# Kernel tuning notes

Measured on AMD Instinct MI355X. Metric: run time of the kernel, lower is better.

The kernel has to match this reference:

```python
import jax, jax.numpy as jnp
import numpy as np

B, S, T = 512, 1024, 48

def setup_inputs() -> dict:
    key = jax.random.key(0)
    k1, k2, k3, k4, k5 = jax.random.split(key, 5)
    emissions = jax.random.normal(k1, (B, S, T), dtype=jnp.float32)
    tags = jax.random.randint(k2, (B, S), 0, T, dtype=jnp.int32)
    mask = jnp.ones((B, S), dtype=jnp.float32)
    transitions = jax.random.normal(k3, (T, T), dtype=jnp.float32)
    start_transitions = jax.random.normal(k4, (T,), dtype=jnp.float32)
    end_transitions = jax.random.normal(k5, (T,), dtype=jnp.float32)
    return {"emissions": emissions, "tags": tags, "mask": mask,
            "transitions": transitions, "start_transitions": start_transitions,
            "end_transitions": end_transitions}

def _crf_loss(emissions, transitions, start_transitions, end_transitions, tags, mask):
    # ---- numerator: score of the gold path (fully vectorized over seq) ----
    emit = jnp.take_along_axis(emissions, tags[..., None], axis=2)[..., 0]  # (B,S)
    trans = transitions[tags[:, 1:], tags[:, :-1]]                          # (B,S-1)
    lengths = jnp.sum(mask, axis=1).astype(jnp.int32)
    last_idx = jnp.clip(lengths - 1, 0)
    last_tags = jnp.take_along_axis(tags, last_idx[:, None], axis=1)[:, 0]
    numerator = (start_transitions[tags[:, 0]] + emit[:, 0]
                 + jnp.sum(mask[:, 1:] * (emit[:, 1:] + trans), axis=1)
                 + end_transitions[last_tags])                               # (B,)

    # ---- denominator: log-partition via forward algorithm (lax.scan) ----
    def step(score, x):
        em_i, m_i = x  # (B,T), (B,)
        # logsumexp over previous tag; emission is prev-independent so add outside
        nxt = jax.nn.logsumexp(score[:, :, None] + transitions.T[None, :, :], axis=1) + em_i
        score = jnp.where(m_i[:, None] > 0, nxt, score)
        return score, None

    init = start_transitions[None, :] + emissions[:, 0]                      # (B,T)
    xs = (jnp.swapaxes(emissions[:, 1:], 0, 1), jnp.swapaxes(mask[:, 1:], 0, 1))
    final, _ = jax.lax.scan(step, init, xs)
    denominator = jax.nn.logsumexp(final + end_transitions[None, :], axis=1)  # (B,)

    return jnp.mean(denominator - numerator)

def reference(emissions, tags, mask, transitions, start_transitions, end_transitions):
    return _crf_loss(emissions, transitions, start_transitions, end_transitions, tags, mask)
```

## Files before the change

kernel.cpp:

```cpp
#include <hip/hip_runtime.h>
#include <math.h>

#define Bn 512
#define Sn 1024
#define Tn 48
#define NSEG 8
#define SEGLEN 128

typedef _Float16 h4 __attribute__((ext_vector_type(4)));
typedef float    f4 __attribute__((ext_vector_type(4)));

static constexpr float LOG2E = 1.4426950408889634f;
static constexpr float LN2f  = 0.6931471805599453f;

#define MFMA16(A, B, C) __builtin_amdgcn_mfma_f32_16x16x16f16((A), (B), (C), 0, 0, 0)

__global__ __launch_bounds__(512)
void crf_fwd_seg(const float* __restrict__ em,
                 const float* __restrict__ mask,
                 const float* __restrict__ trans,
                 const float* __restrict__ startt,
                 const float* __restrict__ endt,
                 float* __restrict__ den_out)
{
  const int b   = blockIdx.x;
  const int tid = threadIdx.x;
  const int wid = tid >> 6;
  const int l   = tid & 63;
  const int c16 = l & 15;
  const int g   = l >> 4;

  __shared__ __align__(16) float Lm[NSEG][48][49];
  __shared__ __align__(16) float mlds[Sn];
  __shared__ float lwbuf[64];

  const float* __restrict__ emb = em + (size_t)b * Sn * Tn;
  const float* __restrict__ mkb = mask + (size_t)b * Sn;

  if (tid < Sn / 4) *(f4*)&mlds[4 * tid] = *(const f4*)(mkb + 4 * tid);

  h4 Afr[3][3];
  float mtg;
  {
    float tl[3][3][4];
    float mt = -1e30f;
    #pragma unroll
    for (int rt = 0; rt < 3; ++rt)
      #pragma unroll
      for (int kt = 0; kt < 3; ++kt) {
        const f4 t4 = *(const f4*)(trans + (16 * rt + c16) * Tn + 16 * kt + 4 * g);
        #pragma unroll
        for (int i = 0; i < 4; ++i) {
          const float v = t4[i] * LOG2E;
          tl[rt][kt][i] = v;
          mt = fmaxf(mt, v);
        }
      }
    #pragma unroll
    for (int off = 1; off < 64; off <<= 1) mt = fmaxf(mt, __shfl_xor(mt, off));
    mtg = mt;
    #pragma unroll
    for (int rt = 0; rt < 3; ++rt)
      #pragma unroll
      for (int kt = 0; kt < 3; ++kt) {
        h4 r;
        #pragma unroll
        for (int i = 0; i < 4; ++i)
          r[i] = (_Float16)__builtin_amdgcn_exp2f(tl[rt][kt][i] - mtg);
        Afr[rt][kt] = r;
      }
  }

  h4 Bfr[3][3];
  float Mc[3] = {0.f, 0.f, 0.f};
  float cnt = 0.f;
  #pragma unroll
  for (int kt = 0; kt < 3; ++kt)
    #pragma unroll
    for (int ct = 0; ct < 3; ++ct) {
      h4 r;
      #pragma unroll
      for (int i = 0; i < 4; ++i)
        r[i] = (_Float16)(((16 * kt + 4 * g + i) == (16 * ct + c16)) ? 1.0f : 0.0f);
      Bfr[kt][ct] = r;
    }

  auto STEP = [&](const f4& e0, const f4& e1, const f4& e2, float mk,
                  float sc0, float sc1, float sc2,
                  float sh0, float sh1, float sh2) {
    f4 eh[3];
    #pragma unroll
    for (int i = 0; i < 4; ++i) {
      eh[0][i] = __builtin_amdgcn_exp2f(fmaf(e0[i], LOG2E, -6.0f));
      eh[1][i] = __builtin_amdgcn_exp2f(fmaf(e1[i], LOG2E, -6.0f));
      eh[2][i] = __builtin_amdgcn_exp2f(fmaf(e2[i], LOG2E, -6.0f));
    }
    f4 acc[3][3];
    #pragma unroll
    for (int rt = 0; rt < 3; ++rt)
      #pragma unroll
      for (int ct = 0; ct < 3; ++ct) acc[rt][ct] = f4{0.f, 0.f, 0.f, 0.f};
    #pragma unroll
    for (int kt = 0; kt < 3; ++kt)
      #pragma unroll
      for (int rt = 0; rt < 3; ++rt)
        #pragma unroll
        for (int ct = 0; ct < 3; ++ct)
          acc[rt][ct] = MFMA16(Afr[rt][kt], Bfr[kt][ct], acc[rt][ct]);
    const float scv[3] = {sc0, sc1, sc2};
    const float shv[3] = {sh0, sh1, sh2};
    const bool on = (mk > 0.0f);
    #pragma unroll
    for (int rt = 0; rt < 3; ++rt)
      #pragma unroll
      for (int ct = 0; ct < 3; ++ct) {
        h4 nb;
        #pragma unroll
        for (int i = 0; i < 4; ++i)
          nb[i] = (_Float16)(acc[rt][ct][i] * eh[rt][i] * scv[ct]);
        Bfr[rt][ct] = on ? nb : Bfr[rt][ct];
      }
    #pragma unroll
    for (int ct = 0; ct < 3; ++ct) Mc[ct] = fmaf(mk, shv[ct], Mc[ct]);
    cnt += mk;
  };

  auto MEASURE = [&](float (&sh)[3], float (&sc)[3]) {
    #pragma unroll
    for (int ct = 0; ct < 3; ++ct) {
      float m = (float)Bfr[0][ct][0];
      #pragma unroll
      for (int rt = 0; rt < 3; ++rt)
        #pragma unroll
        for (int i = 0; i < 4; ++i) m = fmaxf(m, (float)Bfr[rt][ct][i]);
      m = fmaxf(m, __shfl_xor(m, 16));
      m = fmaxf(m, __shfl_xor(m, 32));
      int eb = ((__float_as_int(m) >> 23) & 0xff) - 127;
      eb = eb < -24 ? -24 : (eb > 40 ? 40 : eb);
      sh[ct] = (float)eb;
      sc[ct] = __int_as_float((127 - eb) << 23);
    }
  };

  auto loadE = [&](int s, f4& x, f4& y, f4& z) {
    const float* p = emb + (size_t)s * Tn + 4 * g;
    x = *(const f4*)(p);
    y = *(const f4*)(p + 16);
    z = *(const f4*)(p + 32);
  };

  __syncthreads();

  const int s_begin = 1 + SEGLEN * wid;
  const int nchunk  = (wid == 7) ? 31 : 32;
  float shP[3] = {0.f, 0.f, 0.f}, scP[3] = {1.f, 1.f, 1.f};
  float shA[3] = {0.f, 0.f, 0.f}, scA[3] = {1.f, 1.f, 1.f};

  f4 E0, E1, E2, N0, N1, N2;
  loadE(s_begin, E0, E1, E2);
  int s = s_begin;
  #pragma unroll 1
  for (int c = 0; c < nchunk; ++c) {
    loadE(s + 1, N0, N1, N2);
    STEP(E0, E1, E2, mlds[s], 1.f, 1.f, 1.f, 0.f, 0.f, 0.f);
    loadE(s + 2, E0, E1, E2);
    STEP(N0, N1, N2, mlds[s + 1], scP[0], scP[1], scP[2], shP[0], shP[1], shP[2]);
    MEASURE(shA, scA);
    loadE(s + 3, N0, N1, N2);
    STEP(E0, E1, E2, mlds[s + 2], 1.f, 1.f, 1.f, 0.f, 0.f, 0.f);
    loadE(s + 4, E0, E1, E2);
    STEP(N0, N1, N2, mlds[s + 3], scA[0], scA[1], scA[2], shA[0], shA[1], shA[2]);
    MEASURE(shP, scP);
    s += 4;
  }
  if (wid == 7) {
    loadE(1022, N0, N1, N2);
    STEP(E0, E1, E2, mlds[1021], 1.f, 1.f, 1.f, 0.f, 0.f, 0.f);
    loadE(1023, E0, E1, E2);
    STEP(N0, N1, N2, mlds[1022], scP[0], scP[1], scP[2], shP[0], shP[1], shP[2]);
    MEASURE(shA, scA);
    STEP(E0, E1, E2, mlds[1023], 1.f, 1.f, 1.f, 0.f, 0.f, 0.f);
  }

  const float addc = (mtg + 6.0f) * cnt;
  #pragma unroll
  for (int kt = 0; kt < 3; ++kt)
    #pragma unroll
    for (int ct = 0; ct < 3; ++ct)
      #pragma unroll
      for (int i = 0; i < 4; ++i)
        Lm[wid][16 * kt + 4 * g + i][16 * ct + c16] =
            __builtin_amdgcn_logf((float)Bfr[kt][ct][i]) + Mc[ct] + addc;
  __syncthreads();

  if (wid == 0) {
    float lw = -INFINITY;
    if (l < Tn) lw = (startt[l] + emb[l]) * LOG2E;
    #pragma unroll 1
    for (int sg = 0; sg < NSEG; ++sg) {
      lwbuf[l] = lw;
      float nlw = lw;
      if (l < Tn) {
        float mj = -INFINITY;
        for (int cc = 0; cc < Tn; ++cc)
          mj = fmaxf(mj, Lm[sg][l][cc] + lwbuf[cc]);
        float ssum = 0.f;
        for (int cc = 0; cc < Tn; ++cc)
          ssum += __builtin_amdgcn_exp2f(Lm[sg][l][cc] + lwbuf[cc] - mj);
        nlw = mj + __builtin_amdgcn_logf(ssum);
      }
      lw = nlw;
    }
    float v = (l < Tn) ? lw + endt[l] * LOG2E : -INFINITY;
    float mv = v;
    #pragma unroll
    for (int off = 32; off; off >>= 1) mv = fmaxf(mv, __shfl_xor(mv, off));
    float zz = (l < Tn) ? __builtin_amdgcn_exp2f(v - mv) : 0.f;
    #pragma unroll
    for (int off = 32; off; off >>= 1) zz += __shfl_xor(zz, off);
    if (l == 0) den_out[b] = (mv + __builtin_amdgcn_logf(zz)) * LN2f;
  }
}

__global__ __launch_bounds__(256) void crf_numer(
    const float* __restrict__ em, const int* __restrict__ tags,
    const float* __restrict__ mask, const float* __restrict__ trans,
    const float* __restrict__ startt, const float* __restrict__ endt,
    float* __restrict__ num_out)
{
  const int b = blockIdx.x, t = threadIdx.x;
  const int*   tgb = tags + (size_t)b * Sn;
  const float* mkb = mask + (size_t)b * Sn;
  const float* emb = em + (size_t)b * Sn * Tn;

  const int s0 = t * 4;
  const int4 tg = *(const int4*)(tgb + s0);
  const f4   mk = *(const f4*)(mkb + s0);
  const int  tprev = (t == 0) ? 0 : tgb[s0 - 1];
  const int  tgarr[5] = {tprev, tg.x, tg.y, tg.z, tg.w};

  float acc  = 0.0f;
  float msum = mk[0] + mk[1] + mk[2] + mk[3];
  #pragma unroll
  for (int i = 0; i < 4; ++i) {
    const int s = s0 + i;
    if (s >= 1)
      acc += mk[i] * (emb[(size_t)s * Tn + tgarr[i + 1]] +
                      trans[tgarr[i + 1] * Tn + tgarr[i]]);
  }
  #pragma unroll
  for (int off = 32; off; off >>= 1) {
    acc  += __shfl_xor(acc, off);
    msum += __shfl_xor(msum, off);
  }
  __shared__ float ra[4], rm[4];
  if ((t & 63) == 0) { ra[t >> 6] = acc; rm[t >> 6] = msum; }
  __syncthreads();
  if (t == 0) {
    const float a = ra[0] + ra[1] + ra[2] + ra[3];
    const float m = rm[0] + rm[1] + rm[2] + rm[3];
    int last = (int)(m + 0.5f) - 1;
    if (last < 0) last = 0;
    const int lt = tgb[last];
    const int t0 = tgb[0];
    num_out[b] = startt[t0] + emb[t0] + a + endt[lt];
  }
}

__global__ __launch_bounds__(512) void reduce_loss(const float* __restrict__ den,
                                                   const float* __restrict__ num,
                                                   float* __restrict__ out) {
  __shared__ float red[8];
  const int t = threadIdx.x;
  float v = den[t] - num[t];
  #pragma unroll
  for (int off = 32; off; off >>= 1) v += __shfl_xor(v, off);
  if ((t & 63) == 0) red[t >> 6] = v;
  __syncthreads();
  if (t == 0) {
    float s = 0.f;
    #pragma unroll
    for (int wv = 0; wv < 8; ++wv) s += red[wv];
    out[0] = s * (1.0f / 512.0f);
  }
}

extern "C" void kernel_launch(void* const* d_in, const int* in_sizes, int n_in,
                              void* d_out, int out_size, void* d_ws, size_t ws_size,
                              hipStream_t stream) {
  const float* emissions = (const float*)d_in[0];
  const int*   tags      = (const int*)d_in[1];
  const float* mask      = (const float*)d_in[2];
  const float* trans     = (const float*)d_in[3];
  const float* startt    = (const float*)d_in[4];
  const float* endt      = (const float*)d_in[5];
  float* den_ws = (float*)d_ws;
  float* num_ws = den_ws + Bn;

  crf_numer<<<Bn, 256, 0, stream>>>(emissions, tags, mask, trans, startt, endt, num_ws);
  crf_fwd_seg<<<Bn, 512, 0, stream>>>(emissions, mask, trans, startt, endt, den_ws);
  reduce_loss<<<1, 512, 0, stream>>>(den_ws, num_ws, (float*)d_out);
}
```

Measured before the change: 256.6 us.

## Precompute fp16 exp-emissions in separate pass and use packed half math in recurrence

```diff
diff --git a/kernel.cpp b/kernel.cpp
--- a/kernel.cpp
+++ b/kernel.cpp
@@ -7,6 +7,7 @@
 #define NSEG 8
 #define SEGLEN 128
 
+typedef _Float16 h2 __attribute__((ext_vector_type(2)));
 typedef _Float16 h4 __attribute__((ext_vector_type(4)));
 typedef float    f4 __attribute__((ext_vector_type(4)));
 
@@ -15,12 +16,50 @@
 
 #define MFMA16(A, B, C) __builtin_amdgcn_mfma_f32_16x16x16f16((A), (B), (C), 0, 0, 0)
 
-__global__ __launch_bounds__(512)
+__device__ __forceinline__ h2 hmax2(h2 a, h2 b) {
+#if __has_builtin(__builtin_elementwise_max)
+  return __builtin_elementwise_max(a, b);
+#else
+  h2 r;
+  r[0] = a[0] > b[0] ? a[0] : b[0];
+  r[1] = a[1] > b[1] ? a[1] : b[1];
+  return r;
+#endif
+}
+__device__ __forceinline__ h2 cvt2(float a, float b) {
+  return __builtin_bit_cast(h2, __builtin_amdgcn_cvt_pkrtz(a, b));
+}
+__device__ __forceinline__ h4 mkh4(h2 lo, h2 hi) {
+  return __builtin_shufflevector(lo, hi, 0, 1, 2, 3);
+}
+__device__ __forceinline__ h2 loh(h4 v) { return __builtin_shufflevector(v, v, 0, 1); }
+__device__ __forceinline__ h2 hih(h4 v) { return __builtin_shufflevector(v, v, 2, 3); }
+
+__global__ __launch_bounds__(256) void ehgen(const float* __restrict__ em,
+                                             _Float16* __restrict__ out) {
+  const size_t total = (size_t)Bn * Sn * Tn;
+  const size_t i = ((size_t)blockIdx.x * 256 + threadIdx.x) * 8;
+  if (i >= total) return;
+  const f4 a = *(const f4*)(em + i);
+  const f4 b = *(const f4*)(em + i + 4);
+  h4 o1, o2;
+  #pragma unroll
+  for (int j = 0; j < 4; ++j) {
+    o1[j] = (_Float16)__builtin_amdgcn_exp2f(fmaf(a[j], LOG2E, -6.0f));
+    o2[j] = (_Float16)__builtin_amdgcn_exp2f(fmaf(b[j], LOG2E, -6.0f));
+  }
+  *(h4*)(out + i) = o1;
+  *(h4*)(out + i + 4) = o2;
+}
+
+template <bool PRE>
+__global__ __launch_bounds__(512, 4)
 void crf_fwd_seg(const float* __restrict__ em,
                  const float* __restrict__ mask,
                  const float* __restrict__ trans,
                  const float* __restrict__ startt,
                  const float* __restrict__ endt,
+                 const _Float16* __restrict__ eh16,
                  float* __restrict__ den_out)
 {
   const int b   = blockIdx.x;
@@ -31,13 +70,12 @@
   const int g   = l >> 4;
 
   __shared__ __align__(16) float Lm[NSEG][48][49];
-  __shared__ __align__(16) float mlds[Sn];
   __shared__ float lwbuf[64];
 
-  const float* __restrict__ emb = em + (size_t)b * Sn * Tn;
-  const float* __restrict__ mkb = mask + (size_t)b * Sn;
-
-  if (tid < Sn / 4) *(f4*)&mlds[4 * tid] = *(const f4*)(mkb + 4 * tid);
+  const float*    __restrict__ emb = em + (size_t)b * Sn * Tn;
+  const float*    __restrict__ mkb = mask + (size_t)b * Sn;
+  const _Float16* __restrict__ ehL = PRE ? (eh16 + (size_t)b * Sn * Tn + 4 * g) : nullptr;
+  const float*    __restrict__ emL = emb + 4 * g;
 
   h4 Afr[3][3];
   float mtg;
@@ -85,101 +123,120 @@
       Bfr[kt][ct] = r;
     }
 
-  auto STEP = [&](const f4& e0, const f4& e1, const f4& e2, float mk,
-                  float sc0, float sc1, float sc2,
-                  float sh0, float sh1, float sh2) {
-    f4 eh[3];
-    #pragma unroll
-    for (int i = 0; i < 4; ++i) {
-      eh[0][i] = __builtin_amdgcn_exp2f(fmaf(e0[i], LOG2E, -6.0f));
-      eh[1][i] = __builtin_amdgcn_exp2f(fmaf(e1[i], LOG2E, -6.0f));
-      eh[2][i] = __builtin_amdgcn_exp2f(fmaf(e2[i], LOG2E, -6.0f));
-    }
-    f4 acc[3][3];
-    #pragma unroll
-    for (int rt = 0; rt < 3; ++rt)
-      #pragma unroll
-      for (int ct = 0; ct < 3; ++ct) acc[rt][ct] = f4{0.f, 0.f, 0.f, 0.f};
-    #pragma unroll
-    for (int kt = 0; kt < 3; ++kt)
+  auto STEP = [&](const h4& e0, const h4& e1, const h4& e2, float mkval,
+                  bool APPLY, const float (&scv)[3], const float (&shv)[3]) {
+    if (__int_as_float(__builtin_amdgcn_readfirstlane(__float_as_int(mkval))) > 0.0f) {
+      f4 acc[3][3];
       #pragma unroll
       for (int rt = 0; rt < 3; ++rt)
         #pragma unroll
-        for (int ct = 0; ct < 3; ++ct)
-          acc[rt][ct] = MFMA16(Afr[rt][kt], Bfr[kt][ct], acc[rt][ct]);
-    const float scv[3] = {sc0, sc1, sc2};
-    const float shv[3] = {sh0, sh1, sh2};
-    const bool on = (mk > 0.0f);
-    #pragma unroll
-    for (int rt = 0; rt < 3; ++rt)
-      #pragma unroll
-      for (int ct = 0; ct < 3; ++ct) {
-        h4 nb;
-        #pragma unroll
-        for (int i = 0; i < 4; ++i)
-          nb[i] = (_Float16)(acc[rt][ct][i] * eh[rt][i] * scv[ct]);
-        Bfr[rt][ct] = on ? nb : Bfr[rt][ct];
-      }
-    #pragma unroll
-    for (int ct = 0; ct < 3; ++ct) Mc[ct] = fmaf(mk, shv[ct], Mc[ct]);
-    cnt += mk;
+        for (int ct = 0; ct < 3; ++ct) acc[rt][ct] = f4{0.f, 0.f, 0.f, 0.f};
+      #pragma unroll
+      for (int kt = 0; kt < 3; ++kt)
+        #pragma unroll
+        for (int rt = 0; rt < 3; ++rt)
+          #pragma unroll
+          for (int ct = 0; ct < 3; ++ct)
+            acc[rt][ct] = MFMA16(Afr[rt][kt], Bfr[kt][ct], acc[rt][ct]);
+      const h4 ehv[3] = {e0, e1, e2};
+      #pragma unroll
+      for (int rt = 0; rt < 3; ++rt) {
+        const h2 elo = loh(ehv[rt]);
+        const h2 ehi = hih(ehv[rt]);
+        #pragma unroll
+        for (int ct = 0; ct < 3; ++ct) {
+          f4 a = acc[rt][ct];
+          if (APPLY) {
+            a[0] *= scv[ct]; a[1] *= scv[ct]; a[2] *= scv[ct]; a[3] *= scv[ct];
+          }
+          const h2 lo = cvt2(a[0], a[1]) * elo;
+          const h2 hi = cvt2(a[2], a[3]) * ehi;
+          Bfr[rt][ct] = mkh4(lo, hi);
+        }
+      }
+      if (APPLY) { Mc[0] += shv[0]; Mc[1] += shv[1]; Mc[2] += shv[2]; }
+      cnt += 1.0f;
+    }
   };
 
   auto MEASURE = [&](float (&sh)[3], float (&sc)[3]) {
     #pragma unroll
     for (int ct = 0; ct < 3; ++ct) {
-      float m = (float)Bfr[0][ct][0];
-      #pragma unroll
-      for (int rt = 0; rt < 3; ++rt)
-        #pragma unroll
-        for (int i = 0; i < 4; ++i) m = fmaxf(m, (float)Bfr[rt][ct][i]);
-      m = fmaxf(m, __shfl_xor(m, 16));
-      m = fmaxf(m, __shfl_xor(m, 32));
-      int eb = ((__float_as_int(m) >> 23) & 0xff) - 127;
-      eb = eb < -24 ? -24 : (eb > 40 ? 40 : eb);
+      h2 m = loh(Bfr[0][ct]);
+      m = hmax2(m, hih(Bfr[0][ct]));
+      m = hmax2(m, loh(Bfr[1][ct]));
+      m = hmax2(m, hih(Bfr[1][ct]));
+      m = hmax2(m, loh(Bfr[2][ct]));
+      m = hmax2(m, hih(Bfr[2][ct]));
+      m = hmax2(m, __builtin_bit_cast(h2, __shfl_xor(__builtin_bit_cast(int, m), 16)));
+      m = hmax2(m, __builtin_bit_cast(h2, __shfl_xor(__builtin_bit_cast(int, m), 32)));
+      const float mf = fmaxf((float)m[0], (float)m[1]);
+      int eb = ((__float_as_int(mf) >> 23) & 0xff) - 127;
+      eb = eb < -15 ? -15 : (eb > 15 ? 15 : eb);
       sh[ct] = (float)eb;
       sc[ct] = __int_as_float((127 - eb) << 23);
     }
   };
 
-  auto loadE = [&](int s, f4& x, f4& y, f4& z) {
-    const float* p = emb + (size_t)s * Tn + 4 * g;
-    x = *(const f4*)(p);
-    y = *(const f4*)(p + 16);
-    z = *(const f4*)(p + 32);
+  auto loadEH = [&](int s, h4& x, h4& y, h4& z) {
+    if constexpr (PRE) {
+      const _Float16* p = ehL + (size_t)s * Tn;
+      x = *(const h4*)(p);
+      y = *(const h4*)(p + 16);
+      z = *(const h4*)(p + 32);
+    } else {
+      const float* p = emL + (size_t)s * Tn;
+      const f4 a = *(const f4*)(p);
+      const f4 b2 = *(const f4*)(p + 16);
+      const f4 c2 = *(const f4*)(p + 32);
+      f4 ea, eb2, ec;
+      #pragma unroll
+      for (int i = 0; i < 4; ++i) {
+        ea[i]  = __builtin_amdgcn_exp2f(fmaf(a[i],  LOG2E, -6.0f));
+        eb2[i] = __builtin_amdgcn_exp2f(fmaf(b2[i], LOG2E, -6.0f));
+        ec[i]  = __builtin_amdgcn_exp2f(fmaf(c2[i], LOG2E, -6.0f));
+      }
+      x = mkh4(cvt2(ea[0], ea[1]), cvt2(ea[2], ea[3]));
+      y = mkh4(cvt2(eb2[0], eb2[1]), cvt2(eb2[2], eb2[3]));
+      z = mkh4(cvt2(ec[0], ec[1]), cvt2(ec[2], ec[3]));
+    }
   };
-
-  __syncthreads();
 
   const int s_begin = 1 + SEGLEN * wid;
   const int nchunk  = (wid == 7) ? 31 : 32;
   float shP[3] = {0.f, 0.f, 0.f}, scP[3] = {1.f, 1.f, 1.f};
   float shA[3] = {0.f, 0.f, 0.f}, scA[3] = {1.f, 1.f, 1.f};
-
-  f4 E0, E1, E2, N0, N1, N2;
-  loadE(s_begin, E0, E1, E2);
+  const float sh1[3] = {0.f, 0.f, 0.f};
+  const float sc1[3] = {1.f, 1.f, 1.f};
+
+  h4 E0, E1, E2, N0, N1, N2;
+  f4 mkc = *(const f4*)(mkb + s_begin);
+  f4 mkn;
+  loadEH(s_begin, E0, E1, E2);
   int s = s_begin;
   #pragma unroll 1
   for (int c = 0; c < nchunk; ++c) {
-    loadE(s + 1, N0, N1, N2);
-    STEP(E0, E1, E2, mlds[s], 1.f, 1.f, 1.f, 0.f, 0.f, 0.f);
-    loadE(s + 2, E0, E1, E2);
-    STEP(N0, N1, N2, mlds[s + 1], scP[0], scP[1], scP[2], shP[0], shP[1], shP[2]);
+    mkn = *(const f4*)(mkb + ((c + 1 < nchunk) ? (s + 4) : s));
+    loadEH(s + 1, N0, N1, N2);
+    STEP(E0, E1, E2, mkc[0], false, sc1, sh1);
+    loadEH(s + 2, E0, E1, E2);
+    STEP(N0, N1, N2, mkc[1], true, scP, shP);
     MEASURE(shA, scA);
-    loadE(s + 3, N0, N1, N2);
-    STEP(E0, E1, E2, mlds[s + 2], 1.f, 1.f, 1.f, 0.f, 0.f, 0.f);
-    loadE(s + 4, E0, E1, E2);
-    STEP(N0, N1, N2, mlds[s + 3], scA[0], scA[1], scA[2], shA[0], shA[1], shA[2]);
+    loadEH(s + 3, N0, N1, N2);
+    STEP(E0, E1, E2, mkc[2], false, sc1, sh1);
+    loadEH(s + 4, E0, E1, E2);
+    STEP(N0, N1, N2, mkc[3], true, scA, shA);
     MEASURE(shP, scP);
+    mkc = mkn;
     s += 4;
   }
   if (wid == 7) {
-    loadE(1022, N0, N1, N2);
-    STEP(E0, E1, E2, mlds[1021], 1.f, 1.f, 1.f, 0.f, 0.f, 0.f);
-    loadE(1023, E0, E1, E2);
-    STEP(N0, N1, N2, mlds[1022], scP[0], scP[1], scP[2], shP[0], shP[1], shP[2]);
+    loadEH(1022, N0, N1, N2);
+    STEP(E0, E1, E2, mkb[1021], false, sc1, sh1);
+    loadEH(1023, E0, E1, E2);
+    STEP(N0, N1, N2, mkb[1022], true, scP, shP);
     MEASURE(shA, scA);
-    STEP(E0, E1, E2, mlds[1023], 1.f, 1.f, 1.f, 0.f, 0.f, 0.f);
+    STEP(E0, E1, E2, mkb[1023], false, sc1, sh1);
   }
 
   const float addc = (mtg + 6.0f) * cnt;
@@ -296,8 +353,20 @@
   const float* endt      = (const float*)d_in[5];
   float* den_ws = (float*)d_ws;
   float* num_ws = den_ws + Bn;
+  const size_t ehoff   = 4096;
+  const size_t ehbytes = (size_t)Bn * Sn * Tn * sizeof(_Float16);
+  _Float16* eh16 = (_Float16*)((char*)d_ws + ehoff);
+  const bool pre = (ws_size >= ehoff + ehbytes);
 
   crf_numer<<<Bn, 256, 0, stream>>>(emissions, tags, mask, trans, startt, endt, num_ws);
-  crf_fwd_seg<<<Bn, 512, 0, stream>>>(emissions, mask, trans, startt, endt, den_ws);
+  if (pre) {
+    const int total8 = Bn * Sn * Tn / 8;
+    ehgen<<<(total8 + 255) / 256, 256, 0, stream>>>(emissions, eh16);
+    crf_fwd_seg<true><<<Bn, 512, 0, stream>>>(emissions, mask, trans, startt, endt,
+                                              eh16, den_ws);
+  } else {
+    crf_fwd_seg<false><<<Bn, 512, 0, stream>>>(emissions, mask, trans, startt, endt,
+                                               nullptr, den_ws);
+  }
   reduce_loss<<<1, 512, 0, stream>>>(den_ws, num_ws, (float*)d_out);
 }
```

Result: faster. 208.4 us (-18.8%).
